# Performance work log

Hardware: AMD Instinct MI355X
Metric: run time of the kernel (lower is better)

The kernel has to match this reference:

```python
import jax, jax.numpy as jnp
import numpy as np

TS = 1.5          # hard-coded sampling period in forward()
W_CENTER = 337.927  # hard-coded center frequency in forward()


def shg_mat(yta):
    """Vectorized createSHGmat: yta is a complex64 vector of length N.
    Row m: Ts * fftshift(fft(fftshift(yta * roll(yta, delay[m]) * shiftFactor))).
    torch.roll(x, s)[j] == x[(j - s) % N], matching the gather below."""
    N = yta.shape[0]
    delays_f = jnp.arange(-(N // 2), N // 2, dtype=jnp.float32)
    delays_i = jnp.arange(-(N // 2), N // 2, dtype=jnp.int32)
    shift_factor = jnp.exp(-1j * 2.0 * W_CENTER * TS * delays_f).astype(jnp.complex64)  # [N]
    idx = (jnp.arange(N, dtype=jnp.int32)[None, :] - delays_i[:, None]) % N  # [N, N]
    y_shift = yta[idx]                                    # [N(delay), N(elem)]
    prod = yta[None, :] * y_shift * shift_factor[None, :]  # elementwise, [N, N]
    prod = jnp.fft.fftshift(prod, axes=-1)
    mat = TS * jnp.fft.fftshift(jnp.fft.fft(prod, axis=-1), axes=-1)
    return mat  # complex64 [N, N]


def frog_error(Tref, Tmeas):
    """calcFrogError: scalar FROG error between reference and measured traces."""
    mu = jnp.sum(Tmeas @ Tref) / jnp.sum(Tref @ Tref)
    r = jnp.sum((Tmeas - mu * Tref) ** 2)
    norm = jnp.float32(Tmeas.size) * jnp.max(Tmeas) ** 2
    return jnp.sqrt(r / norm)


def setup_inputs() -> dict:
    key = jax.random.key(0)
    k1, k2, k3 = jax.random.split(key, 3)
    B, N = 8, 1024
    prediction = jax.random.normal(k1, (B, 2 * N), dtype=jnp.float32)
    label = jax.random.normal(k2, (B, 2 * N), dtype=jnp.float32)
    spectrogram = jax.random.uniform(k3, (N, N), dtype=jnp.float32)
    return {"prediction": prediction, "label": label, "spectrogram": spectrogram}


def reference(prediction, label, spectrogram):
    B, two_n = prediction.shape
    n = two_n // 2
    pred_analytical = (prediction[:, :n] + 1j * prediction[:, n:]).astype(jnp.complex64)  # [B, N]
    mats = jax.vmap(shg_mat)(pred_analytical)          # [B, N, N] complex64
    Tref = jnp.abs(mats)                               # predicted SHG trace magnitude
    errs = jax.vmap(lambda t: frog_error(t, spectrogram))(Tref)  # [B]
    # loss = (sum over batch of frog_error) / batch_size; masked MSE terms in the
    # original are computed but never added to the returned loss, so they are omitted.
    return jnp.mean(errs)
```

## Files before the change

kernel.cpp:

```cpp
#include <hip/hip_runtime.h>
#include <math.h>

#define N 1024
#define B_ 8
#define T_ 256
#define NREP 4
#define CHUNKS 64

#define OFF_SF      0
#define OFF_TA      2048
#define OFF_TB      6144
#define OFF_ROWSUM  6272
#define ZERO_START  14464
#define OFF_COLSUMM 14464
#define OFF_SUMM2   15488
#define OFF_MAXM    15489
#define OFF_SUMMT   15496
#define OFF_SUMTT   15504
#define OFF_COLT    15520
#define WS_END      (OFF_COLT + B_ * NREP * N)

__device__ __forceinline__ float wave_sum(float v) {
    #pragma unroll
    for (int o = 32; o > 0; o >>= 1) v += __shfl_down(v, o, 64);
    return v;
}
__device__ __forceinline__ float wave_max(float v) {
    #pragma unroll
    for (int o = 32; o > 0; o >>= 1) v = fmaxf(v, __shfl_down(v, o, 64));
    return v;
}

__device__ __forceinline__ void cmul(float& xr, float& xi, float wr, float wi) {
    float r = xr * wr - xi * wi;
    float i = xr * wi + xi * wr;
    xr = r; xi = i;
}

__device__ __forceinline__ void dft4(float& r0, float& i0, float& r1, float& i1,
                                     float& r2, float& i2, float& r3, float& i3) {
    float e0r = r0 + r2, e0i = i0 + i2;
    float e1r = r0 - r2, e1i = i0 - i2;
    float e2r = r1 + r3, e2i = i1 + i3;
    float e3r = r1 - r3, e3i = i1 - i3;
    r0 = e0r + e2r; i0 = e0i + e2i;
    r2 = e0r - e2r; i2 = e0i - e2i;
    r1 = e1r + e3i; i1 = e1i - e3r;
    r3 = e1r - e3i; i3 = e1i + e3r;
}

__device__ __forceinline__ void dft16(float xr[16], float xi[16]) {
    #pragma unroll
    for (int b = 0; b < 4; ++b)
        dft4(xr[b], xi[b], xr[4 + b], xi[4 + b], xr[8 + b], xi[8 + b], xr[12 + b], xi[12 + b]);
    const float C1 = 0.9238795325112867f, S1 = 0.3826834323650898f;
    const float C2 = 0.7071067811865476f;
    cmul(xr[5],  xi[5],   C1, -S1);
    cmul(xr[6],  xi[6],   C2, -C2);
    cmul(xr[7],  xi[7],   S1, -C1);
    cmul(xr[9],  xi[9],   C2, -C2);
    { float t = xr[10]; xr[10] = xi[10]; xi[10] = -t; }
    cmul(xr[11], xi[11], -C2, -C2);
    cmul(xr[13], xi[13],  S1, -C1);
    cmul(xr[14], xi[14], -C2, -C2);
    cmul(xr[15], xi[15], -C1,  S1);
    #pragma unroll
    for (int c = 0; c < 4; ++c)
        dft4(xr[4 * c], xi[4 * c], xr[4 * c + 1], xi[4 * c + 1],
             xr[4 * c + 2], xi[4 * c + 2], xr[4 * c + 3], xi[4 * c + 3]);
}

template<int CTRL>
__device__ __forceinline__ float dppf(float x) {
    return __int_as_float(__builtin_amdgcn_update_dpp(
        0, __float_as_int(x), CTRL, 0xF, 0xF, true));
}
#define DPP_XOR1 0xB1
#define DPP_XOR2 0x4E

__global__ __launch_bounds__(T_) void k_prep(float* ws, float* out) {
    const int e = blockIdx.x * T_ + threadIdx.x;
    if (e < 1024) {
        double ang = -2.0 * 337.927 * 1.5 * (double)(e - 512);
        double s, c;
        sincos(ang, &s, &c);
        ws[OFF_SF + 2 * e]     = (float)c;
        ws[OFF_SF + 2 * e + 1] = (float)s;
    } else if (e < 2048) {
        int e2 = e - 1024;
        int k1 = e2 >> 6, uu = e2 & 63;
        double ang = -2.0 * M_PI * (double)(uu * k1) / 1024.0;
        double s, c;
        sincos(ang, &s, &c);
        ws[OFF_TA + 2 * e2]     = (float)c;
        ws[OFF_TA + 2 * e2 + 1] = (float)s;
    } else if (e < 2112) {
        int e2 = e - 2048;
        int k2 = e2 >> 2, n3 = e2 & 3;
        double ang = -2.0 * M_PI * (double)(n3 * k2) / 64.0;
        double s, c;
        sincos(ang, &s, &c);
        ws[OFF_TB + 2 * e2]     = (float)c;
        ws[OFF_TB + 2 * e2 + 1] = (float)s;
    }
    for (int j = ZERO_START + e; j < WS_END; j += 12 * T_) ws[j] = 0.f;
    if (e == 0) out[0] = 0.f;
}

__global__ __launch_bounds__(T_, 3) void k_row(const float* __restrict__ pred,
                                               const float* __restrict__ M,
                                               float* __restrict__ ws) {
    __shared__ float2 Y2[N];
    __shared__ float2 Ysf2[N];
    __shared__ float2 TP[4][N];
    __shared__ float2 TB2[64];
    __shared__ float red[2][4];
    const int t = threadIdx.x;
    const int cnk = blockIdx.x;
    const int b = blockIdx.y;
    const int wid = t >> 6, u = t & 63;

    if (b == B_) {
        const int r0 = cnk * 16;
        float cs0 = 0.f, cs1 = 0.f, cs2 = 0.f, cs3 = 0.f, sq = 0.f, mx = 0.f;
        for (int r = 0; r < 16; ++r) {
            const float* row = M + (size_t)(r0 + r) * N;
            float v0 = row[t], v1 = row[t + 256], v2 = row[t + 512], v3 = row[t + 768];
            cs0 += v0; cs1 += v1; cs2 += v2; cs3 += v3;
            sq += v0 * v0 + v1 * v1 + v2 * v2 + v3 * v3;
            mx = fmaxf(mx, fmaxf(fmaxf(v0, v1), fmaxf(v2, v3)));
        }
        atomicAdd(&ws[OFF_COLSUMM + t],       cs0);
        atomicAdd(&ws[OFF_COLSUMM + t + 256], cs1);
        atomicAdd(&ws[OFF_COLSUMM + t + 512], cs2);
        atomicAdd(&ws[OFF_COLSUMM + t + 768], cs3);
        sq = wave_sum(sq);
        mx = wave_max(mx);
        if (u == 0) { red[0][wid] = sq; red[1][wid] = mx; }
        __syncthreads();
        if (t == 0) {
            atomicAdd(&ws[OFF_SUMM2], red[0][0] + red[0][1] + red[0][2] + red[0][3]);
            float X = fmaxf(fmaxf(red[1][0], red[1][1]), fmaxf(red[1][2], red[1][3]));
            atomicMax((unsigned int*)ws + OFF_MAXM, __float_as_uint(X));
        }
        return;
    }

    {
        const float* pr = pred + (size_t)b * 2 * N;
        float4 re = *(const float4*)(pr + 4 * t);
        float4 im = *(const float4*)(pr + N + 4 * t);
        const float4* sfp = (const float4*)(ws + OFF_SF);
        float4 sA = sfp[2 * t], sB = sfp[2 * t + 1];
        int j0 = 4 * t;
        Y2[j0 + 0] = make_float2(re.x, im.x);
        Y2[j0 + 1] = make_float2(re.y, im.y);
        Y2[j0 + 2] = make_float2(re.z, im.z);
        Y2[j0 + 3] = make_float2(re.w, im.w);
        Ysf2[j0 + 0] = make_float2(re.x * sA.x - im.x * sA.y, re.x * sA.y + im.x * sA.x);
        Ysf2[j0 + 1] = make_float2(re.y * sA.z - im.y * sA.w, re.y * sA.w + im.y * sA.z);
        Ysf2[j0 + 2] = make_float2(re.z * sB.x - im.z * sB.y, re.z * sB.y + im.z * sB.x);
        Ysf2[j0 + 3] = make_float2(re.w * sB.z - im.w * sB.w, re.w * sB.w + im.w * sB.z);
        if (t < 64) TB2[t] = ((const float2*)(ws + OFF_TB))[t];
    }
    float tar[16], tai[16];
    {
        const float2* taT = (const float2*)(ws + OFF_TA);
        #pragma unroll
        for (int r = 1; r < 16; ++r) {
            int k1 = ((r & 3) << 2) | (r >> 2);
            float2 wv = taT[(k1 << 6) + u];
            tar[r] = wv.x; tai[r] = wv.y;
        }
    }
    __syncthreads();

    const int k1u = u >> 2;
    const int n3 = u & 3;
    const int k3 = ((u & 1) << 1) | ((u >> 1) & 1);
    const int clane = (k1u | (k3 << 8)) ^ 512;
    const bool hi2 = (u & 2) != 0;
    const bool odd = (u & 1) != 0;
    float2* tp = TP[wid];

    float colr[16];
    #pragma unroll
    for (int r = 0; r < 16; ++r) colr[r] = 0.f;
    float mtl = 0.f, ttl = 0.f;

    const int base = cnk * 8 + wid * 2;
    const int nrow = (cnk == CHUNKS - 1 && wid == 0) ? 3 : 2;

    for (int rr = 0; rr < nrow; ++rr) {
        const int m = (rr < 2) ? (base + rr) : 512;
        const int mm = (N - m) & (N - 1);
        const float w = (mm == m) ? 1.f : 2.f;

        float xr[16], xi[16];
        const int sbase = (u - m + 512) & (N - 1);
        #pragma unroll
        for (int n1 = 0; n1 < 16; ++n1) {
            float2 a = Ysf2[(n1 << 6) + u];
            int s = (sbase + (n1 << 6)) & (N - 1);
            float2 yb = Y2[s];
            xr[n1] = a.x * yb.x - a.y * yb.y;
            xi[n1] = a.x * yb.y + a.y * yb.x;
        }
        dft16(xr, xi);
        #pragma unroll
        for (int r = 1; r < 16; ++r) cmul(xr[r], xi[r], tar[r], tai[r]);

        asm volatile("s_waitcnt lgkmcnt(0)" ::: "memory");
        #pragma unroll
        for (int r = 0; r < 16; ++r) {
            int k1 = ((r & 3) << 2) | (r >> 2);
            int el = (k1 << 6) | (((k1u ^ k1) & 15) << 2) | n3;
            tp[el] = make_float2(xr[r], xi[r]);
        }
        asm volatile("s_waitcnt lgkmcnt(0)" ::: "memory");
        #pragma unroll
        for (int n2 = 0; n2 < 16; ++n2) {
            int el = (k1u << 6) | (((n2 ^ k1u) & 15) << 2) | n3;
            float2 v = tp[el];
            xr[n2] = v.x; xi[n2] = v.y;
        }

        dft16(xr, xi);
        #pragma unroll
        for (int r = 1; r < 16; ++r) {
            int k2 = ((r & 3) << 2) | (r >> 2);
            float2 wv = TB2[(k2 << 2) | n3];
            cmul(xr[r], xi[r], wv.x, wv.y);
        }

        const float* Mrow  = M + (size_t)m * N + clane;
        const float* Mrow2 = M + (size_t)mm * N + clane;
        const bool domm = (mm != m);
        const float w225 = w * 2.25f;
        float rs = 0.f;
        #pragma unroll
        for (int r = 0; r < 16; ++r) {
            int k2 = ((r & 3) << 2) | (r >> 2);
            float ar = xr[r], ai = xi[r];
            float br = dppf<DPP_XOR2>(ar), bi = dppf<DPP_XOR2>(ai);
            float zr = hi2 ? (br - ar) : (ar + br);
            float zi = hi2 ? (bi - ai) : (ai + bi);
            float qr = dppf<DPP_XOR1>(zr), qi = dppf<DPP_XOR1>(zi);
            float Xr = odd ? (qr - (hi2 ? zi : zr)) : (zr + (hi2 ? qi : qr));
            float Xi = odd ? (qi + (hi2 ? zr : -zi)) : (zi + (hi2 ? -qr : qi));
            float mag2 = Xr * Xr + Xi * Xi;
            float v = 1.5f * sqrtf(mag2);
            rs  += v;
            ttl += w225 * mag2;
            float ms = Mrow[k2 << 4];
            if (domm) ms += Mrow2[k2 << 4];
            mtl += ms * v;
            colr[r] += w * v;
        }
        rs = wave_sum(rs);
        if (u == 0) {
            ws[OFF_ROWSUM + (size_t)b * N + m] = rs;
            if (mm != m) ws[OFF_ROWSUM + (size_t)b * N + mm] = rs;
        }
    }

    mtl = wave_sum(mtl);
    ttl = wave_sum(ttl);
    if (u == 0) {
        atomicAdd(&ws[OFF_SUMMT + b], mtl);
        atomicAdd(&ws[OFF_SUMTT + b], ttl);
    }
    float* colT = ws + OFF_COLT + (size_t)(b * NREP + (cnk & (NREP - 1))) * N;
    #pragma unroll
    for (int r = 0; r < 16; ++r) {
        int k2 = ((r & 3) << 2) | (r >> 2);
        atomicAdd(&colT[clane + (k2 << 4)], colr[r]);
    }
}

__global__ __launch_bounds__(T_) void k_final(float* ws, float* out) {
    __shared__ double redn[4], redd[4];
    const int b = blockIdx.x;
    const int t = threadIdx.x;
    const int wid = t >> 6, lane = t & 63;
    const float* rowsum = ws + OFF_ROWSUM + (size_t)b * N;
    double num = 0.0, den = 0.0;
    #pragma unroll
    for (int q = 0; q < 4; ++q) {
        int j = t + 256 * q;
        double r = (double)rowsum[j];
        float ct = 0.f;
        #pragma unroll
        for (int rep = 0; rep < NREP; ++rep)
            ct += ws[OFF_COLT + (size_t)(b * NREP + rep) * N + j];
        num += (double)ws[OFF_COLSUMM + j] * r;
        den += (double)ct * r;
    }
    #pragma unroll
    for (int o = 32; o > 0; o >>= 1) {
        num += __shfl_down(num, o, 64);
        den += __shfl_down(den, o, 64);
    }
    if (lane == 0) { redn[wid] = num; redd[wid] = den; }
    __syncthreads();
    if (t == 0) {
        double NUM = redn[0] + redn[1] + redn[2] + redn[3];
        double DEN = redd[0] + redd[1] + redd[2] + redd[3];
        double mu = NUM / DEN;
        double r = (double)ws[OFF_SUMM2] - 2.0 * mu * (double)ws[OFF_SUMMT + b]
                 + mu * mu * (double)ws[OFF_SUMTT + b];
        float mx = ws[OFF_MAXM];
        double norm = 1048576.0 * (double)mx * (double)mx;
        atomicAdd(out, (float)(sqrt(r / norm) / 8.0));
    }
}

extern "C" void kernel_launch(void* const* d_in, const int* in_sizes, int n_in,
                              void* d_out, int out_size, void* d_ws, size_t ws_size,
                              hipStream_t stream) {
    const float* pred = (const float*)d_in[0];
    const float* M = (const float*)d_in[2];
    float* ws = (float*)d_ws;
    float* out = (float*)d_out;

    k_prep<<<12, T_, 0, stream>>>(ws, out);
    dim3 grid(CHUNKS, B_ + 1);
    k_row<<<grid, T_, 0, stream>>>(pred, M, ws);
    k_final<<<B_, T_, 0, stream>>>(ws, out);
}
```

Measured before the change: 121.3 us.

## Use 512-thread row blocks with one row per wave and fused spectrogram stats

Doubles the k_row block to 512 threads so each wave handles one mirrored row pair instead of two. The separate extra grid row that reduced spectrogram statistics is removed; the batch-0 blocks now compute column sums, sum of squares and max from the M values they already load. The shared-memory Ysf2 precompute and the per-thread twiddle registers are dropped in favour of on-the-fly loads, which should cut register and LDS pressure to allow higher occupancy. In exchange, column sums are now issued as per-element atomics for every row, and block-level reductions go through shared memory, which adds atomic traffic and a sync.

```diff
diff --git a/kernel.cpp b/kernel.cpp
--- a/kernel.cpp
+++ b/kernel.cpp
@@ -3,7 +3,7 @@
 
 #define N 1024
 #define B_ 8
-#define T_ 256
+#define T_ 512
 #define NREP 4
 #define CHUNKS 64
 
@@ -78,8 +78,8 @@
 #define DPP_XOR1 0xB1
 #define DPP_XOR2 0x4E
 
-__global__ __launch_bounds__(T_) void k_prep(float* ws, float* out) {
-    const int e = blockIdx.x * T_ + threadIdx.x;
+__global__ __launch_bounds__(256) void k_prep(float* ws, float* out) {
+    const int e = blockIdx.x * 256 + threadIdx.x;
     if (e < 1024) {
         double ang = -2.0 * 337.927 * 1.5 * (double)(e - 512);
         double s, c;
@@ -103,75 +103,29 @@
         ws[OFF_TB + 2 * e2]     = (float)c;
         ws[OFF_TB + 2 * e2 + 1] = (float)s;
     }
-    for (int j = ZERO_START + e; j < WS_END; j += 12 * T_) ws[j] = 0.f;
+    for (int j = ZERO_START + e; j < WS_END; j += 12 * 256) ws[j] = 0.f;
     if (e == 0) out[0] = 0.f;
 }
 
-__global__ __launch_bounds__(T_, 3) void k_row(const float* __restrict__ pred,
+__global__ __launch_bounds__(T_, 4) void k_row(const float* __restrict__ pred,
                                                const float* __restrict__ M,
                                                float* __restrict__ ws) {
     __shared__ float2 Y2[N];
-    __shared__ float2 Ysf2[N];
-    __shared__ float2 TP[4][N];
+    __shared__ float2 TP[8][N];
     __shared__ float2 TB2[64];
-    __shared__ float red[2][4];
+    __shared__ float redf[4][8];
     const int t = threadIdx.x;
     const int cnk = blockIdx.x;
     const int b = blockIdx.y;
     const int wid = t >> 6, u = t & 63;
 
-    if (b == B_) {
-        const int r0 = cnk * 16;
-        float cs0 = 0.f, cs1 = 0.f, cs2 = 0.f, cs3 = 0.f, sq = 0.f, mx = 0.f;
-        for (int r = 0; r < 16; ++r) {
-            const float* row = M + (size_t)(r0 + r) * N;
-            float v0 = row[t], v1 = row[t + 256], v2 = row[t + 512], v3 = row[t + 768];
-            cs0 += v0; cs1 += v1; cs2 += v2; cs3 += v3;
-            sq += v0 * v0 + v1 * v1 + v2 * v2 + v3 * v3;
-            mx = fmaxf(mx, fmaxf(fmaxf(v0, v1), fmaxf(v2, v3)));
-        }
-        atomicAdd(&ws[OFF_COLSUMM + t],       cs0);
-        atomicAdd(&ws[OFF_COLSUMM + t + 256], cs1);
-        atomicAdd(&ws[OFF_COLSUMM + t + 512], cs2);
-        atomicAdd(&ws[OFF_COLSUMM + t + 768], cs3);
-        sq = wave_sum(sq);
-        mx = wave_max(mx);
-        if (u == 0) { red[0][wid] = sq; red[1][wid] = mx; }
-        __syncthreads();
-        if (t == 0) {
-            atomicAdd(&ws[OFF_SUMM2], red[0][0] + red[0][1] + red[0][2] + red[0][3]);
-            float X = fmaxf(fmaxf(red[1][0], red[1][1]), fmaxf(red[1][2], red[1][3]));
-            atomicMax((unsigned int*)ws + OFF_MAXM, __float_as_uint(X));
-        }
-        return;
-    }
-
     {
         const float* pr = pred + (size_t)b * 2 * N;
-        float4 re = *(const float4*)(pr + 4 * t);
-        float4 im = *(const float4*)(pr + N + 4 * t);
-        const float4* sfp = (const float4*)(ws + OFF_SF);
-        float4 sA = sfp[2 * t], sB = sfp[2 * t + 1];
-        int j0 = 4 * t;
-        Y2[j0 + 0] = make_float2(re.x, im.x);
-        Y2[j0 + 1] = make_float2(re.y, im.y);
-        Y2[j0 + 2] = make_float2(re.z, im.z);
-        Y2[j0 + 3] = make_float2(re.w, im.w);
-        Ysf2[j0 + 0] = make_float2(re.x * sA.x - im.x * sA.y, re.x * sA.y + im.x * sA.x);
-        Ysf2[j0 + 1] = make_float2(re.y * sA.z - im.y * sA.w, re.y * sA.w + im.y * sA.z);
-        Ysf2[j0 + 2] = make_float2(re.z * sB.x - im.z * sB.y, re.z * sB.y + im.z * sB.x);
-        Ysf2[j0 + 3] = make_float2(re.w * sB.z - im.w * sB.w, re.w * sB.w + im.w * sB.z);
+        float2 re = *(const float2*)(pr + 2 * t);
+        float2 im = *(const float2*)(pr + N + 2 * t);
+        Y2[2 * t]     = make_float2(re.x, im.x);
+        Y2[2 * t + 1] = make_float2(re.y, im.y);
         if (t < 64) TB2[t] = ((const float2*)(ws + OFF_TB))[t];
-    }
-    float tar[16], tai[16];
-    {
-        const float2* taT = (const float2*)(ws + OFF_TA);
-        #pragma unroll
-        for (int r = 1; r < 16; ++r) {
-            int k1 = ((r & 3) << 2) | (r >> 2);
-            float2 wv = taT[(k1 << 6) + u];
-            tar[r] = wv.x; tai[r] = wv.y;
-        }
     }
     __syncthreads();
 
@@ -182,33 +136,59 @@
     const bool hi2 = (u & 2) != 0;
     const bool odd = (u & 1) != 0;
     float2* tp = TP[wid];
-
-    float colr[16];
-    #pragma unroll
-    for (int r = 0; r < 16; ++r) colr[r] = 0.f;
-    float mtl = 0.f, ttl = 0.f;
-
-    const int base = cnk * 8 + wid * 2;
-    const int nrow = (cnk == CHUNKS - 1 && wid == 0) ? 3 : 2;
+    const float2* sf2 = (const float2*)(ws + OFF_SF);
+    const float2* taT = (const float2*)(ws + OFF_TA);
+
+    float mtl = 0.f, ttl = 0.f, sql = 0.f, mxl = 0.f;
+    const bool dostats = (b == 0);
+    const int nrow = (cnk == 0 && wid == 0) ? 2 : 1;
 
     for (int rr = 0; rr < nrow; ++rr) {
-        const int m = (rr < 2) ? (base + rr) : 512;
+        const int m = (rr == 0) ? (cnk * 8 + wid) : 512;
         const int mm = (N - m) & (N - 1);
-        const float w = (mm == m) ? 1.f : 2.f;
+        const bool domm = (mm != m);
+        const float w = domm ? 2.f : 1.f;
+
+        const float* Mrow  = M + (size_t)m * N + clane;
+        const float* Mrow2 = M + (size_t)mm * N + clane;
+        float mr[16], mr2[16];
+        #pragma unroll
+        for (int r = 0; r < 16; ++r) {
+            int k2 = ((r & 3) << 2) | (r >> 2);
+            mr[r] = Mrow[k2 << 4];
+        }
+        if (domm) {
+            #pragma unroll
+            for (int r = 0; r < 16; ++r) {
+                int k2 = ((r & 3) << 2) | (r >> 2);
+                mr2[r] = Mrow2[k2 << 4];
+            }
+        } else {
+            #pragma unroll
+            for (int r = 0; r < 16; ++r) mr2[r] = 0.f;
+        }
 
         float xr[16], xi[16];
         const int sbase = (u - m + 512) & (N - 1);
         #pragma unroll
         for (int n1 = 0; n1 < 16; ++n1) {
-            float2 a = Ysf2[(n1 << 6) + u];
+            int j = (n1 << 6) + u;
+            float2 yj = Y2[j];
+            float2 sv = sf2[j];
             int s = (sbase + (n1 << 6)) & (N - 1);
             float2 yb = Y2[s];
-            xr[n1] = a.x * yb.x - a.y * yb.y;
-            xi[n1] = a.x * yb.y + a.y * yb.x;
+            float ar = yj.x * sv.x - yj.y * sv.y;
+            float ai = yj.x * sv.y + yj.y * sv.x;
+            xr[n1] = ar * yb.x - ai * yb.y;
+            xi[n1] = ar * yb.y + ai * yb.x;
         }
         dft16(xr, xi);
         #pragma unroll
-        for (int r = 1; r < 16; ++r) cmul(xr[r], xi[r], tar[r], tai[r]);
+        for (int r = 1; r < 16; ++r) {
+            int k1 = ((r & 3) << 2) | (r >> 2);
+            float2 wv = taT[(k1 << 6) + u];
+            cmul(xr[r], xi[r], wv.x, wv.y);
+        }
 
         asm volatile("s_waitcnt lgkmcnt(0)" ::: "memory");
         #pragma unroll
@@ -233,9 +213,7 @@
             cmul(xr[r], xi[r], wv.x, wv.y);
         }
 
-        const float* Mrow  = M + (size_t)m * N + clane;
-        const float* Mrow2 = M + (size_t)mm * N + clane;
-        const bool domm = (mm != m);
+        float* colT = ws + OFF_COLT + (size_t)(b * NREP + (cnk & (NREP - 1))) * N;
         const float w225 = w * 2.25f;
         float rs = 0.f;
         #pragma unroll
@@ -252,33 +230,44 @@
             float v = 1.5f * sqrtf(mag2);
             rs  += v;
             ttl += w225 * mag2;
-            float ms = Mrow[k2 << 4];
-            if (domm) ms += Mrow2[k2 << 4];
+            float ms = mr[r] + mr2[r];
             mtl += ms * v;
-            colr[r] += w * v;
+            atomicAdd(&colT[clane + (k2 << 4)], w * v);
+            if (dostats) {
+                sql += mr[r] * mr[r] + mr2[r] * mr2[r];
+                mxl = fmaxf(mxl, fmaxf(mr[r], mr2[r]));
+                atomicAdd(&ws[OFF_COLSUMM + clane + (k2 << 4)], ms);
+            }
         }
         rs = wave_sum(rs);
         if (u == 0) {
             ws[OFF_ROWSUM + (size_t)b * N + m] = rs;
-            if (mm != m) ws[OFF_ROWSUM + (size_t)b * N + mm] = rs;
+            if (domm) ws[OFF_ROWSUM + (size_t)b * N + mm] = rs;
         }
     }
 
     mtl = wave_sum(mtl);
     ttl = wave_sum(ttl);
-    if (u == 0) {
-        atomicAdd(&ws[OFF_SUMMT + b], mtl);
-        atomicAdd(&ws[OFF_SUMTT + b], ttl);
-    }
-    float* colT = ws + OFF_COLT + (size_t)(b * NREP + (cnk & (NREP - 1))) * N;
-    #pragma unroll
-    for (int r = 0; r < 16; ++r) {
-        int k2 = ((r & 3) << 2) | (r >> 2);
-        atomicAdd(&colT[clane + (k2 << 4)], colr[r]);
-    }
-}
-
-__global__ __launch_bounds__(T_) void k_final(float* ws, float* out) {
+    if (dostats) { sql = wave_sum(sql); mxl = wave_max(mxl); }
+    if (u == 0) { redf[0][wid] = mtl; redf[1][wid] = ttl; redf[2][wid] = sql; redf[3][wid] = mxl; }
+    __syncthreads();
+    if (t == 0) {
+        float smt = 0.f, stt = 0.f, ssq = 0.f, smx = 0.f;
+        #pragma unroll
+        for (int i = 0; i < 8; ++i) {
+            smt += redf[0][i]; stt += redf[1][i];
+            ssq += redf[2][i]; smx = fmaxf(smx, redf[3][i]);
+        }
+        atomicAdd(&ws[OFF_SUMMT + b], smt);
+        atomicAdd(&ws[OFF_SUMTT + b], stt);
+        if (dostats) {
+            atomicAdd(&ws[OFF_SUMM2], ssq);
+            atomicMax((unsigned int*)ws + OFF_MAXM, __float_as_uint(smx));
+        }
+    }
+}
+
+__global__ __launch_bounds__(256) void k_final(float* ws, float* out) {
     __shared__ double redn[4], redd[4];
     const int b = blockIdx.x;
     const int t = threadIdx.x;
@@ -323,8 +312,8 @@
     float* ws = (float*)d_ws;
     float* out = (float*)d_out;
 
-    k_prep<<<12, T_, 0, stream>>>(ws, out);
-    dim3 grid(CHUNKS, B_ + 1);
+    k_prep<<<12, 256, 0, stream>>>(ws, out);
+    dim3 grid(CHUNKS, B_);
     k_row<<<grid, T_, 0, stream>>>(pred, M, ws);
-    k_final<<<B_, T_, 0, stream>>>(ws, out);
-}
+    k_final<<<B_, 256, 0, stream>>>(ws, out);
+}
```

Measured after the change: 172.3 us. 42.0% more time.
